# Performance work log

Measured on AMD Instinct MI355X. Metric: run time of the kernel, lower is better.

## Reference

```python
import jax, jax.numpy as jnp
import numpy as np

LN_EPS = 1e-5
TOP_K = 2

def _layer_norm(x, g, b):
    m = jnp.mean(x, axis=-1, keepdims=True)
    v = jnp.var(x, axis=-1, keepdims=True)
    return (x - m) * jax.lax.rsqrt(v + LN_EPS) * g + b

def _skew(X, pad_value):
    # shift every row one step right: [B,M,L] -> [B,M,M+L]
    B, M, L = X.shape
    X = jnp.pad(X, ((0, 0), (0, 0), (0, M + 1)), constant_values=pad_value)
    X = X.reshape(B, -1)[:, :-M]
    return X.reshape(B, M, M + L)

def _unskew(X):
    # reverse of _skew: [B,M,M+L] -> [B,M,L]
    B, M, Lt = X.shape
    L = Lt - M
    X = X.reshape(B, -1)
    X = jnp.pad(X, ((0, 0), (0, M)))
    return X.reshape(B, M, M + L + 1)[:, :, :L]

def _heads(x, K, D):
    # [B,T,H] -> [B*K,T,D]
    B, T, _ = x.shape
    return x.reshape(B, T, K, D).transpose(0, 2, 1, 3).reshape(B * K, T, D)

def setup_inputs() -> dict:
    key = jax.random.key(0)
    ks = jax.random.split(key, 12)
    B, M, L, H, Dh, E, Kh = 4, 512, 512, 1024, 2048, 8, 8
    D = H // Kh
    s = 0.02
    return {
        "h": jax.random.normal(ks[0], (B, M, H), jnp.float32),
        "h_cache": jax.random.normal(ks[1], (B, L, H), jnp.float32),
        "key_pe": jax.random.normal(ks[2], (1, D, L), jnp.float32) * s,
        "Wq": jax.random.normal(ks[3], (H, H), jnp.float32) * s,
        "Wk": jax.random.normal(ks[4], (H, H), jnp.float32) * s,
        "Wv": jax.random.normal(ks[5], (H, H), jnp.float32) * s,
        "Wo": jax.random.normal(ks[6], (H, H), jnp.float32) * s,
        "ln1_g": jnp.ones((H,), jnp.float32),
        "ln1_b": jnp.zeros((H,), jnp.float32),
        "gate_W": jax.random.normal(ks[7], (H, E), jnp.float32) * s,
        "gate_b": jnp.zeros((E,), jnp.float32),
        "W1": jax.random.normal(ks[8], (E, H, Dh), jnp.float32) * s,
        "b1": jnp.zeros((E, Dh), jnp.float32),
        "W2": jax.random.normal(ks[9], (E, Dh, H), jnp.float32) * s,
        "b2": jnp.zeros((E, H), jnp.float32),
        "ln2_g": jnp.ones((H,), jnp.float32),
        "ln2_b": jnp.zeros((H,), jnp.float32),
    }

def reference(h, h_cache, key_pe, Wq, Wk, Wv, Wo, ln1_g, ln1_b,
              gate_W, gate_b, W1, b1, W2, b2, ln2_g, ln2_b):
    B, M, H = h.shape
    L = h_cache.shape[1]
    Kh = 8
    D = H // Kh
    # --- multi-head relative-position attention over (cache, current) ---
    h_all = jnp.concatenate([h_cache, h], axis=1)            # [B, L+M, H]
    q = _heads(h @ Wq, Kh, D)                                # [B*K, M, D]
    k = _heads(h_all @ Wk, Kh, D)                            # [B*K, M+L, D]
    v = _heads(h_all @ Wv, Kh, D)                            # [B*K, M+L, D]
    attn_cont = _unskew(jnp.einsum('bmd,bnd->bmn', q, k))    # [B*K, M, L]
    attn_pos = jnp.einsum('bmd,xdl->bml', q, key_pe)         # [B*K, M, L]
    attn = jax.nn.softmax((attn_cont + attn_pos) / jnp.sqrt(jnp.float32(D)), axis=-1)
    out = jnp.einsum('bmn,bnd->bmd', _skew(attn, 0.0), v)    # [B*K, M, D]
    out = out.reshape(B, Kh, M, D).transpose(0, 2, 1, 3).reshape(B, M, H)
    attn_out = out @ Wo
    h1 = _layer_norm(h + attn_out, ln1_g, ln1_b)             # post-LN residual
    # --- top-k gated MoE FFN (NaiveGate), post-LN residual ---
    x = h1.reshape(-1, H)                                    # [N, H]
    N = x.shape[0]
    E = gate_b.shape[0]
    logits = x @ gate_W + gate_b                             # [N, E]
    top_val, top_idx = jax.lax.top_k(logits, TOP_K)          # [N, k]
    scores = jax.nn.softmax(top_val, axis=-1)                # [N, k]
    combine = jnp.zeros((N, E), x.dtype).at[jnp.arange(N)[:, None], top_idx].add(scores)
    he = jax.nn.relu(jnp.einsum('nh,ehf->enf', x, W1) + b1[:, None, :])  # [E, N, Dh]
    ye = jnp.einsum('enf,efh->enh', he, W2) + b2[:, None, :]             # [E, N, H]
    core = jnp.einsum('ne,enh->nh', combine, ye).reshape(B, M, H)
    output = _layer_norm(h1 + core, ln2_g, ln2_b)
    return output, top_idx
```

## Files before the change

### kernel.cpp

```cpp
#include <hip/hip_runtime.h>
#include <hip/hip_bf16.h>
#include <stdint.h>


typedef _Float16 f16;
typedef _Float16 f16x8 __attribute__((ext_vector_type(8)));
typedef _Float16 f16x4 __attribute__((ext_vector_type(4)));
typedef float    f32x4 __attribute__((ext_vector_type(4)));
typedef int      i32x4 __attribute__((ext_vector_type(4)));

#define MFMA16(a, b, c) __builtin_amdgcn_mfma_f32_16x16x32_f16((a), (b), (c), 0, 0, 0)
#define LO_SCALE 2048.0f
#define LO_INV   4.8828125e-4f

__device__ __forceinline__ void split2(float x, f16* h, f16* l) {
  f16 hh = (f16)x;
  *h = hh;
  *l = (f16)((x - (float)hh) * LO_SCALE);
}

__device__ __forceinline__ f32x4 zero4() {
  f32x4 z; z[0] = 0.f; z[1] = 0.f; z[2] = 0.f; z[3] = 0.f; return z;
}

__device__ __forceinline__ void gload_lds16(const void* g, void* l) {
  __builtin_amdgcn_global_load_lds((__attribute__((address_space(1))) void*)g,
                                   (__attribute__((address_space(3))) void*)l,
                                   16, 0, 0);
}

__global__ void __launch_bounds__(256) cast_hall_k(const float* __restrict__ h,
                                                   const float* __restrict__ hc,
                                                   f16* __restrict__ hi,
                                                   f16* __restrict__ lo) {
  int c = blockIdx.x * 256 + threadIdx.x;
  int e0 = c * 8;
  int row = e0 >> 10;
  int col = e0 & 1023;
  int b = row >> 10, pos = row & 1023;
  const float* src = (pos < 512) ? (hc + (size_t)((b << 9) + pos) * 1024 + col)
                                 : (h  + (size_t)((b << 9) + (pos - 512)) * 1024 + col);
  float4 v0 = ((const float4*)src)[0];
  float4 v1 = ((const float4*)src)[1];
  float xs[8] = {v0.x, v0.y, v0.z, v0.w, v1.x, v1.y, v1.z, v1.w};
  f16x8 vh, vl;
#pragma unroll
  for (int i = 0; i < 8; i++) { f16 a, bb; split2(xs[i], &a, &bb); vh[i] = a; vl[i] = bb; }
  *(f16x8*)&hi[e0] = vh;
  *(f16x8*)&lo[e0] = vl;
}

template <int SPLIT>
__global__ void __launch_bounds__(256) wprep_k(const float* __restrict__ in,
                                               f16* __restrict__ oh,
                                               f16* __restrict__ ol,
                                               int K, int N) {
  in += (size_t)blockIdx.z * K * N;
  oh += (size_t)blockIdx.z * K * N;
  if constexpr (SPLIT) ol += (size_t)blockIdx.z * K * N;
  __shared__ float tile[32][33];
  const int n0 = blockIdx.x * 32, k0 = blockIdx.y * 32;
  {
    int r = threadIdx.x >> 3, c4 = (threadIdx.x & 7) * 4;
    float4 v = *(const float4*)&in[(size_t)(k0 + r) * N + n0 + c4];
    tile[r][c4 + 0] = v.x; tile[r][c4 + 1] = v.y;
    tile[r][c4 + 2] = v.z; tile[r][c4 + 3] = v.w;
  }
  __syncthreads();
  int t = threadIdx.x;
  if constexpr (!SPLIT) { if (t >= 128) return; }
  int half = SPLIT ? (t >> 7) : 0;
  int r = t & 127;
  int nt = r >> 6, lane = r & 63;
  int lr = lane & 15, lgp = lane >> 4;
  f16x8 v;
#pragma unroll
  for (int j = 0; j < 8; j++) {
    float x = tile[lgp * 8 + j][nt * 16 + lr];
    f16 hh, ll; split2(x, &hh, &ll);
    v[j] = half ? ll : hh;
  }
  size_t blob = (((size_t)(n0 >> 4) + nt) * (K >> 5) + (k0 >> 5)) * 512 + lane * 8;
  f16* dst = half ? ol : oh;
  *(f16x8*)&dst[blob] = v;
}

template <int SPLIT>
__global__ void __launch_bounds__(256) transpose_cast_k(const float* __restrict__ in,
                                                        f16* __restrict__ oh,
                                                        f16* __restrict__ ol,
                                                        int R, int C) {
  in += (size_t)blockIdx.z * R * C;
  oh += (size_t)blockIdx.z * R * C;
  if constexpr (SPLIT) ol += (size_t)blockIdx.z * R * C;
  __shared__ float tile[32][33];
  int c0 = blockIdx.x * 32, r0 = blockIdx.y * 32;
  int tr = threadIdx.x >> 3, tc = (threadIdx.x & 7) * 4;
  float4 v = *(const float4*)&in[(size_t)(r0 + tr) * C + c0 + tc];
  tile[tr][tc + 0] = v.x; tile[tr][tc + 1] = v.y; tile[tr][tc + 2] = v.z; tile[tr][tc + 3] = v.w;
  __syncthreads();
  int oc = tr;
  int orr = tc;
  f16x4 vh, vl;
#pragma unroll
  for (int i = 0; i < 4; i++) {
    float x = tile[orr + i][oc];
    f16 a, bb; split2(x, &a, &bb);
    vh[i] = a; vl[i] = bb;
  }
  *(f16x4*)&oh[(size_t)(c0 + oc) * R + r0 + orr] = vh;
  if constexpr (SPLIT) *(f16x4*)&ol[(size_t)(c0 + oc) * R + r0 + orr] = vl;
}

#define AM_ID 0
#define AM_GA 2
#define AM_PA 3
#define EP_QKV 0
#define EP_F32 2
#define EP_HE 3
#define EP_YE 4

template <int SPLIT, int BM, int BN, int AMAP, int EPI>
__global__ void __launch_bounds__(256) gemm_k(
    const f16* __restrict__ Ah, const f16* __restrict__ Al,
    const f16* __restrict__ Bh, const f16* __restrict__ Bl,
    void* __restrict__ o0, void* __restrict__ o1,
    const float* __restrict__ bias,
    int Kd, int strideA, int bExpStride,
    const int* __restrict__ list, const int* __restrict__ bases,
    const int* __restrict__ counts) {
  constexpr int PL = SPLIT ? 2 : 1;
  constexpr int MT = BM / 32;
  constexpr int NT = BN / 32;
  constexpr int AIT = BM / 64;
  const int e = blockIdx.z;
  int cnt = 0, base0 = 0;
  if constexpr (AMAP == AM_GA || AMAP == AM_PA) {
    cnt = counts[e]; base0 = bases[e];
    if ((int)blockIdx.y * BM >= cnt) return;
    Bh += (size_t)e * bExpStride;
    if constexpr (SPLIT) Bl += (size_t)e * bExpStride;
  }
  __shared__ f16 sA[PL][BM * 32];
  const int n0 = blockIdx.x * BN, r0 = blockIdx.y * BM;
  const int tid = threadIdx.x, lane = tid & 63, wv = tid >> 6;
  const int wm = (wv >> 1) * (BM / 2), wn = (wv & 1) * (BN / 2);
  const int bKt = Kd >> 5;
  const int gnt0 = (n0 + wn) >> 4;

  f32x4 accM[MT][NT], accC[MT][NT];
#pragma unroll
  for (int i = 0; i < MT; i++)
#pragma unroll
    for (int j = 0; j < NT; j++) { accM[i][j] = zero4(); accC[i][j] = zero4(); }

  int aRow[AIT], aCu[AIT];
#pragma unroll
  for (int c = 0; c < AIT; c++) {
    int u = c * 256 + tid;
    int r = u >> 2, cu = u & 3;
    aCu[c] = ((cu ^ ((r >> 1) & 3)) << 3);
    int rr = r0 + r;
    int g;
    if constexpr (AMAP == AM_ID) g = rr;
    else if constexpr (AMAP == AM_GA) g = (rr < cnt) ? list[base0 + rr] : 0;
    else g = base0 + rr;
    aRow[c] = g;
  }

  for (int k0 = 0; k0 < Kd; k0 += 32) {
    const int kt = k0 >> 5;
    f16x8 bh[NT], bl[NT];
#pragma unroll
    for (int nt = 0; nt < NT; nt++) {
      size_t bi = ((size_t)(gnt0 + nt) * bKt + kt) * 512 + lane * 8;
      bh[nt] = *(const f16x8*)&Bh[bi];
      if constexpr (SPLIT) bl[nt] = *(const f16x8*)&Bl[bi];
    }
#pragma unroll
    for (int c = 0; c < AIT; c++) {
      int u = c * 256 + tid;
      gload_lds16(&Ah[(size_t)aRow[c] * strideA + k0 + aCu[c]], &sA[0][u * 8]);
      if constexpr (SPLIT)
        gload_lds16(&Al[(size_t)aRow[c] * strideA + k0 + aCu[c]], &sA[1][u * 8]);
    }
    __syncthreads();

    f16x8 ah[MT], al[MT];
#pragma unroll
    for (int mt = 0; mt < MT; mt++) {
      int r = wm + mt * 16 + (lane & 15);
      int cu = (lane >> 4) ^ ((r >> 1) & 3);
      ah[mt] = *(const f16x8*)&sA[0][(r * 4 + cu) * 8];
      if constexpr (SPLIT) al[mt] = *(const f16x8*)&sA[1][(r * 4 + cu) * 8];
    }
#pragma unroll
    for (int nt = 0; nt < NT; nt++) {
#pragma unroll
      for (int mt = 0; mt < MT; mt++) {
        accM[mt][nt] = MFMA16(ah[mt], bh[nt], accM[mt][nt]);
        if constexpr (SPLIT) {
          accC[mt][nt] = MFMA16(ah[mt], bl[nt], accC[mt][nt]);
          accC[mt][nt] = MFMA16(al[mt], bh[nt], accC[mt][nt]);
        }
      }
    }
    __syncthreads();
  }

#pragma unroll
  for (int mt = 0; mt < MT; mt++)
#pragma unroll
    for (int nt = 0; nt < NT; nt++)
#pragma unroll
      for (int rg = 0; rg < 4; rg++) {
        int row = r0 + wm + mt * 16 + ((lane >> 4) << 2) + rg;
        int col = n0 + wn + nt * 16 + (lane & 15);
        float v = accM[mt][nt][rg];
        if constexpr (SPLIT) v += accC[mt][nt][rg] * LO_INV;
        if constexpr (EPI == EP_QKV) {
          f16* QH = (f16*)o0;
          f16* QL = QH + (1u << 21);
          f16* KH = QL + (1u << 21);
          f16* KL = KH + (1u << 22);
          f16* VTH = KL + (1u << 22);
          f16* VTL = VTH + (1u << 22);
          int b = row >> 10, pos = row & 1023;
          int seg = col >> 10, hd = (col >> 7) & 7, d = col & 127;
          f16 hh, ll; split2(v, &hh, &ll);
          if (seg == 0) {
            if (pos >= 512) {
              size_t ad = ((size_t)((((b << 3) + hd) << 9) + (pos - 512))) * 128 + d;
              QH[ad] = hh; QL[ad] = ll;
            }
          } else if (seg == 1) {
            size_t ad = ((size_t)((((b << 3) + hd) << 10) + pos)) * 128 + d;
            KH[ad] = hh; KL[ad] = ll;
          } else {
            size_t ad = ((size_t)((((b << 3) + hd) << 7) + d)) * 1024 + pos;
            VTH[ad] = hh; VTL[ad] = ll;
          }
        } else if constexpr (EPI == EP_F32) {
          ((float*)o0)[(size_t)row * 1024 + col] = v;
        } else if constexpr (EPI == EP_HE) {
          if (row < cnt) {
            float t = v + bias[(e << 11) + col];
            ((f16*)o0)[(size_t)(base0 + row) * 2048 + col] = (f16)fmaxf(t, 0.f);
          }
        } else if constexpr (EPI == EP_YE) {
          if (row < cnt)
            ((float*)o0)[(size_t)(base0 + row) * 1024 + col] = v + bias[(e << 10) + col];
        }
      }
}

__device__ __forceinline__ void unpack_p(const unsigned* sp, f16x8* hi, f16x8* lo) {
  i32x4 u0 = *(const i32x4*)sp;
  i32x4 u1 = *(const i32x4*)(sp + 4);
  i32x4 h, l;
  h[0] = (u0[0] & 0xffff) | (u0[1] << 16);
  h[1] = (u0[2] & 0xffff) | (u0[3] << 16);
  h[2] = (u1[0] & 0xffff) | (u1[1] << 16);
  h[3] = (u1[2] & 0xffff) | (u1[3] << 16);
  l[0] = (int)(((unsigned)u0[0] >> 16) | ((unsigned)u0[1] & 0xffff0000u));
  l[1] = (int)(((unsigned)u0[2] >> 16) | ((unsigned)u0[3] & 0xffff0000u));
  l[2] = (int)(((unsigned)u1[0] >> 16) | ((unsigned)u1[1] & 0xffff0000u));
  l[3] = (int)(((unsigned)u1[2] >> 16) | ((unsigned)u1[3] & 0xffff0000u));
  *hi = __builtin_bit_cast(f16x8, h);
  *lo = __builtin_bit_cast(f16x8, l);
}

__global__ void __launch_bounds__(256) attn_k(
    const f16* __restrict__ qh_, const f16* __restrict__ ql_,
    const f16* __restrict__ kh_, const f16* __restrict__ kl_,
    const f16* __restrict__ ph_, const f16* __restrict__ pl_,
    const f16* __restrict__ vh_, const f16* __restrict__ vl_,
    f16* __restrict__ oh_, f16* __restrict__ ol_) {
  __shared__ float S[32][548];
  const int bh = blockIdx.y;
  const int m0 = blockIdx.x * 32;
  const int tid = threadIdx.x, lane = tid & 63, wv = tid >> 6;
  const int lr = lane & 15, lgp = lane >> 4;

  f16x8 qh[2][4], ql[2][4];
  {
    const size_t qbase = ((size_t)bh * 512 + m0) * 128;
#pragma unroll
    for (int mt = 0; mt < 2; mt++)
#pragma unroll
      for (int kb = 0; kb < 4; kb++) {
        size_t off = qbase + (size_t)(mt * 16 + lr) * 128 + kb * 32 + lgp * 8;
        qh[mt][kb] = *(const f16x8*)&qh_[off];
        ql[mt][kb] = *(const f16x8*)&ql_[off];
      }
  }

  {
    const size_t kbase = ((size_t)bh * 1024 + m0) * 128;
    int ntB = (wv < 2) ? wv * 9 : 18 + (wv - 2) * 8;
    int ntE = ntB + ((wv < 2) ? 9 : 8);
    for (int nt = ntB; nt < ntE; ++nt) {
      f16x8 kh[4], kl[4];
#pragma unroll
      for (int kb = 0; kb < 4; kb++) {
        size_t off = kbase + (size_t)(nt * 16 + lr) * 128 + kb * 32 + lgp * 8;
        kh[kb] = *(const f16x8*)&kh_[off];
        kl[kb] = *(const f16x8*)&kl_[off];
      }
      f32x4 aM[2], aC[2];
      aM[0] = zero4(); aM[1] = zero4(); aC[0] = zero4(); aC[1] = zero4();
#pragma unroll
      for (int kb = 0; kb < 4; kb++)
#pragma unroll
        for (int mt = 0; mt < 2; mt++) {
          aM[mt] = MFMA16(qh[mt][kb], kh[kb], aM[mt]);
          aC[mt] = MFMA16(qh[mt][kb], kl[kb], aC[mt]);
          aC[mt] = MFMA16(ql[mt][kb], kh[kb], aC[mt]);
        }
#pragma unroll
      for (int mt = 0; mt < 2; mt++)
#pragma unroll
        for (int rg = 0; rg < 4; rg++) {
          int m = mt * 16 + lgp * 4 + rg;
          S[m][nt * 16 + lr] = aM[mt][rg] + aC[mt][rg] * LO_INV;
        }
    }
  }
  __syncthreads();

  {
    for (int lt = wv * 8; lt < wv * 8 + 8; ++lt) {
      f16x8 eh[4], el[4];
#pragma unroll
      for (int kb = 0; kb < 4; kb++) {
        size_t off = (size_t)(lt * 16 + lr) * 128 + kb * 32 + lgp * 8;
        eh[kb] = *(const f16x8*)&ph_[off];
        el[kb] = *(const f16x8*)&pl_[off];
      }
      f32x4 aM[2], aC[2];
      aM[0] = zero4(); aM[1] = zero4(); aC[0] = zero4(); aC[1] = zero4();
#pragma unroll
      for (int kb = 0; kb < 4; kb++)
#pragma unroll
        for (int mt = 0; mt < 2; mt++) {
          aM[mt] = MFMA16(qh[mt][kb], eh[kb], aM[mt]);
          aC[mt] = MFMA16(qh[mt][kb], el[kb], aC[mt]);
          aC[mt] = MFMA16(ql[mt][kb], eh[kb], aC[mt]);
        }
#pragma unroll
      for (int mt = 0; mt < 2; mt++)
#pragma unroll
        for (int rg = 0; rg < 4; rg++) {
          int m = mt * 16 + lgp * 4 + rg;
          int lc = lt * 16 + lr;
          S[m][m + lc] += aM[mt][rg] + aC[mt][rg] * LO_INV;
        }
    }
  }
  __syncthreads();

  {
    const float scl = 0.08838834764831843f;
    for (int rr = 0; rr < 8; ++rr) {
      int m = wv * 8 + rr;
      float mx = -3.0e38f;
#pragma unroll
      for (int it = 0; it < 9; ++it) {
        int j = it * 64 + lane;
        if (j < 544 && j >= m && j < m + 512) mx = fmaxf(mx, S[m][j]);
      }
#pragma unroll
      for (int o = 32; o > 0; o >>= 1) mx = fmaxf(mx, __shfl_xor(mx, o));
      float pv[9]; float sm = 0.f;
#pragma unroll
      for (int it = 0; it < 9; ++it) {
        int j = it * 64 + lane;
        float p = 0.f;
        if (j < 544 && j >= m && j < m + 512) p = expf((S[m][j] - mx) * scl);
        pv[it] = p; sm += p;
      }
#pragma unroll
      for (int o = 32; o > 0; o >>= 1) sm += __shfl_xor(sm, o);
      float inv = 1.0f / sm;
#pragma unroll
      for (int it = 0; it < 9; ++it) {
        int j = it * 64 + lane;
        if (j < 544) {
          float pn = pv[it] * inv;
          f16 hh, ll; split2(pn, &hh, &ll);
          unsigned pk = (unsigned)__builtin_bit_cast(unsigned short, hh) |
                        ((unsigned)__builtin_bit_cast(unsigned short, ll) << 16);
          ((unsigned*)&S[m][0])[j] = pk;
        }
      }
    }
  }
  __syncthreads();

  f32x4 accM[2][2], accC[2][2];
#pragma unroll
  for (int i = 0; i < 2; i++)
#pragma unroll
    for (int j = 0; j < 2; j++) { accM[i][j] = zero4(); accC[i][j] = zero4(); }
  for (int kb = 0; kb < 17; ++kb) {
    f16x8 pah[2], pal[2];
#pragma unroll
    for (int mt = 0; mt < 2; mt++) {
      const unsigned* sp = (const unsigned*)&S[mt * 16 + lr][0] + kb * 32 + lgp * 8;
      unpack_p(sp, &pah[mt], &pal[mt]);
    }
#pragma unroll
    for (int ntl = 0; ntl < 2; ++ntl) {
      int d = wv * 32 + ntl * 16 + lr;
      size_t off = ((size_t)bh * 128 + d) * 1024 + m0 + kb * 32 + lgp * 8;
      f16x8 vh = *(const f16x8*)&vh_[off];
      f16x8 vl = *(const f16x8*)&vl_[off];
#pragma unroll
      for (int mt = 0; mt < 2; mt++) {
        accM[mt][ntl] = MFMA16(pah[mt], vh, accM[mt][ntl]);
        accC[mt][ntl] = MFMA16(pah[mt], vl, accC[mt][ntl]);
        accC[mt][ntl] = MFMA16(pal[mt], vh, accC[mt][ntl]);
      }
    }
  }
  const int b = bh >> 3, hd = bh & 7;
#pragma unroll
  for (int mt = 0; mt < 2; mt++)
#pragma unroll
    for (int ntl = 0; ntl < 2; ntl++)
#pragma unroll
      for (int rg = 0; rg < 4; rg++) {
        int m = mt * 16 + lgp * 4 + rg;
        int d = wv * 32 + ntl * 16 + lr;
        float v = accM[mt][ntl][rg] + accC[mt][ntl][rg] * LO_INV;
        size_t ad = ((size_t)(b * 512 + m0 + m)) * 1024 + hd * 128 + d;
        f16 hh, ll; split2(v, &hh, &ll);
        oh_[ad] = hh; ol_[ad] = ll;
      }
}

__device__ __forceinline__ float blk_sum(float v, float* red) {
#pragma unroll
  for (int o = 32; o > 0; o >>= 1) v += __shfl_xor(v, o);
  int wv = threadIdx.x >> 6;
  if ((threadIdx.x & 63) == 0) red[wv] = v;
  __syncthreads();
  float r = red[0] + red[1] + red[2] + red[3];
  __syncthreads();
  return r;
}

__global__ void __launch_bounds__(256) ln1_k(const float* __restrict__ h,
                                             const float* __restrict__ ap,
                                             const float* __restrict__ g,
                                             const float* __restrict__ bb,
                                             float* __restrict__ h1,
                                             f16* __restrict__ h1h) {
  int row = blockIdx.x;
  __shared__ float red[4];
  float4 hv = ((const float4*)(h + (size_t)row * 1024))[threadIdx.x];
  float4 av = ((const float4*)(ap + (size_t)row * 1024))[threadIdx.x];
  float4 x; x.x = hv.x + av.x; x.y = hv.y + av.y; x.z = hv.z + av.z; x.w = hv.w + av.w;
  float s = x.x + x.y + x.z + x.w;
  s = blk_sum(s, red);
  float mean = s * (1.0f / 1024.0f);
  float4 d; d.x = x.x - mean; d.y = x.y - mean; d.z = x.z - mean; d.w = x.w - mean;
  float s2 = d.x * d.x + d.y * d.y + d.z * d.z + d.w * d.w;
  s2 = blk_sum(s2, red);
  float var = s2 * (1.0f / 1024.0f);
  float inv = 1.0f / sqrtf(var + 1e-5f);
  float4 gv = ((const float4*)g)[threadIdx.x];
  float4 bv = ((const float4*)bb)[threadIdx.x];
  float4 y; y.x = d.x * inv * gv.x + bv.x; y.y = d.y * inv * gv.y + bv.y;
  y.z = d.z * inv * gv.z + bv.z; y.w = d.w * inv * gv.w + bv.w;
  ((float4*)(h1 + (size_t)row * 1024))[threadIdx.x] = y;
  f16x4 yh; yh[0] = (f16)y.x; yh[1] = (f16)y.y; yh[2] = (f16)y.z; yh[3] = (f16)y.w;
  *(f16x4*)&h1h[(size_t)row * 1024 + threadIdx.x * 4] = yh;
}

__global__ void __launch_bounds__(256) gate_k(const float* __restrict__ h1,
                                              const float* __restrict__ gW,
                                              const float* __restrict__ gb,
                                              float* __restrict__ outIdx,
                                              float* __restrict__ sc,
                                              int* __restrict__ te,
                                              int* __restrict__ ctrl) {
  int t = blockIdx.x * 4 + (threadIdx.x >> 6);
  int lane = threadIdx.x & 63;
  float a0 = 0, a1 = 0, a2 = 0, a3 = 0, a4 = 0, a5 = 0, a6 = 0, a7 = 0;
  for (int i = lane; i < 1024; i += 64) {
    float x = h1[(size_t)t * 1024 + i];
    const float4* w = (const float4*)&gW[i * 8];
    float4 w0 = w[0], w1 = w[1];
    a0 += x * w0.x; a1 += x * w0.y; a2 += x * w0.z; a3 += x * w0.w;
    a4 += x * w1.x; a5 += x * w1.y; a6 += x * w1.z; a7 += x * w1.w;
  }
  float av[8] = {a0, a1, a2, a3, a4, a5, a6, a7};
#pragma unroll
  for (int e = 0; e < 8; e++)
#pragma unroll
    for (int o = 32; o > 0; o >>= 1) av[e] += __shfl_xor(av[e], o);
  if (lane == 0) {
#pragma unroll
    for (int e = 0; e < 8; e++) av[e] += gb[e];
    int i0 = 0; float v0 = av[0];
#pragma unroll
    for (int e = 1; e < 8; e++) if (av[e] > v0) { v0 = av[e]; i0 = e; }
    int i1 = -1; float v1 = -3.0e38f;
#pragma unroll
    for (int e = 0; e < 8; e++) if (e != i0 && av[e] > v1) { v1 = av[e]; i1 = e; }
    float ex = expf(v1 - v0);
    float den = 1.0f + ex;
    outIdx[t * 2] = (float)i0; outIdx[t * 2 + 1] = (float)i1;
    sc[t * 2] = 1.0f / den; sc[t * 2 + 1] = ex / den;
    te[t * 2] = i0; te[t * 2 + 1] = i1;
    atomicAdd(&ctrl[i0], 1); atomicAdd(&ctrl[i1], 1);
  }
}

__global__ void scan_k(int* ctrl) {
  if (threadIdx.x == 0 && blockIdx.x == 0) {
    int s = 0;
    for (int e = 0; e < 8; e++) { ctrl[8 + e] = s; s += ctrl[e]; }
  }
}

__global__ void __launch_bounds__(256) scatter_k(const int* __restrict__ te,
                                                 int* ctrl,
                                                 int* __restrict__ list,
                                                 int* __restrict__ ppos) {
  int t = blockIdx.x * 256 + threadIdx.x;
  if (t >= 2048) return;
#pragma unroll
  for (int s = 0; s < 2; s++) {
    int e = te[t * 2 + s];
    int pos = atomicAdd(&ctrl[16 + e], 1);
    int pr = ctrl[8 + e] + pos;
    list[pr] = t;
    ppos[t * 2 + s] = pr;
  }
}

__global__ void __launch_bounds__(256) comb_ln2_k(const float* __restrict__ h1,
                                                  const float* __restrict__ ye,
                                                  const float* __restrict__ sc,
                                                  const int* __restrict__ ppos,
                                                  const float* __restrict__ g,
                                                  const float* __restrict__ bb,
                                                  float* __restrict__ out) {
  int row = blockIdx.x;
  __shared__ float red[4];
  int p0 = ppos[row * 2], p1 = ppos[row * 2 + 1];
  float s0 = sc[row * 2], s1 = sc[row * 2 + 1];
  float4 a = ((const float4*)(h1 + (size_t)row * 1024))[threadIdx.x];
  float4 y0 = ((const float4*)(ye + (size_t)p0 * 1024))[threadIdx.x];
  float4 y1 = ((const float4*)(ye + (size_t)p1 * 1024))[threadIdx.x];
  float4 x;
  x.x = a.x + s0 * y0.x + s1 * y1.x; x.y = a.y + s0 * y0.y + s1 * y1.y;
  x.z = a.z + s0 * y0.z + s1 * y1.z; x.w = a.w + s0 * y0.w + s1 * y1.w;
  float s = x.x + x.y + x.z + x.w;
  s = blk_sum(s, red);
  float mean = s * (1.0f / 1024.0f);
  float4 d; d.x = x.x - mean; d.y = x.y - mean; d.z = x.z - mean; d.w = x.w - mean;
  float s2 = d.x * d.x + d.y * d.y + d.z * d.z + d.w * d.w;
  s2 = blk_sum(s2, red);
  float var = s2 * (1.0f / 1024.0f);
  float inv = 1.0f / sqrtf(var + 1e-5f);
  float4 gv = ((const float4*)g)[threadIdx.x];
  float4 bv = ((const float4*)bb)[threadIdx.x];
  float4 y; y.x = d.x * inv * gv.x + bv.x; y.y = d.y * inv * gv.y + bv.y;
  y.z = d.z * inv * gv.z + bv.z; y.w = d.w * inv * gv.w + bv.w;
  ((float4*)(out + (size_t)row * 1024))[threadIdx.x] = y;
}

extern "C" void kernel_launch(void* const* d_in, const int* in_sizes, int n_in,
                              void* d_out, int out_size, void* d_ws, size_t ws_size,
                              hipStream_t stream) {
  const float* h   = (const float*)d_in[0];
  const float* hc  = (const float*)d_in[1];
  const float* pe  = (const float*)d_in[2];
  const float* Wq  = (const float*)d_in[3];
  const float* Wk  = (const float*)d_in[4];
  const float* Wv  = (const float*)d_in[5];
  const float* Wo  = (const float*)d_in[6];
  const float* g1  = (const float*)d_in[7];
  const float* b1n = (const float*)d_in[8];
  const float* gW  = (const float*)d_in[9];
  const float* gb  = (const float*)d_in[10];
  const float* W1  = (const float*)d_in[11];
  const float* b1e = (const float*)d_in[12];
  const float* W2  = (const float*)d_in[13];
  const float* b2e = (const float*)d_in[14];
  const float* g2  = (const float*)d_in[15];
  const float* b2n = (const float*)d_in[16];
  float* out = (float*)d_out;
  float* outIdx = out + 2097152;

  char* w = (char*)d_ws;
  size_t off = 0;
  auto alloc = [&](size_t bytes) -> char* {
    char* p = w + off;
    off += (bytes + 255) & ~(size_t)255;
    return p;
  };
  int*   ctrl    = (int*)alloc(128);
  f16*   hallH   = (f16*)alloc(4096ull * 1024 * 2);
  f16*   hallL   = (f16*)alloc(4096ull * 1024 * 2);
  f16*   WqkvtH  = (f16*)alloc(3072ull * 1024 * 2);
  f16*   WqkvtL  = (f16*)alloc(3072ull * 1024 * 2);
  f16*   WotH    = (f16*)alloc(1024ull * 1024 * 2);
  f16*   WotL    = (f16*)alloc(1024ull * 1024 * 2);
  f16*   peH     = (f16*)alloc(512ull * 128 * 2);
  f16*   peL     = (f16*)alloc(512ull * 128 * 2);
  f16*   qkv     = (f16*)alloc(20971520ull * 2);
  f16*   qH  = qkv;
  f16*   qL  = qH + (1u << 21);
  f16*   kH  = qL + (1u << 21);
  f16*   kL  = kH + (1u << 22);
  f16*   vtH = kL + (1u << 22);
  f16*   vtL = vtH + (1u << 22);
  f16*   attH  = (f16*)alloc(2097152ull * 2);
  f16*   attL  = (f16*)alloc(2097152ull * 2);
  float* aproj = (float*)alloc(2097152ull * 4);
  float* h1    = (float*)alloc(2097152ull * 4);
  f16*   h1h   = (f16*)alloc(2097152ull * 2);
  f16*   W1t   = (f16*)alloc(16777216ull * 2);
  f16*   W2t   = (f16*)alloc(16777216ull * 2);
  f16*   he    = (f16*)alloc(4224ull * 2048 * 2);
  float* ye    = (float*)alloc(4224ull * 1024 * 4);
  float* scb   = (float*)alloc(2048ull * 2 * 4);
  int*   te    = (int*)alloc(2048ull * 2 * 4);
  int*   ppos  = (int*)alloc(2048ull * 2 * 4);
  int*   list  = (int*)alloc(4096ull * 4);
  (void)in_sizes; (void)n_in; (void)out_size; (void)ws_size;

  hipMemsetAsync(ctrl, 0, 128, stream);

  cast_hall_k<<<2048, 256, 0, stream>>>(h, hc, hallH, hallL);
  wprep_k<1><<<dim3(32, 32, 1), 256, 0, stream>>>(Wq, WqkvtH, WqkvtL, 1024, 1024);
  wprep_k<1><<<dim3(32, 32, 1), 256, 0, stream>>>(Wk, WqkvtH + 1048576, WqkvtL + 1048576, 1024, 1024);
  wprep_k<1><<<dim3(32, 32, 1), 256, 0, stream>>>(Wv, WqkvtH + 2097152, WqkvtL + 2097152, 1024, 1024);
  wprep_k<1><<<dim3(32, 32, 1), 256, 0, stream>>>(Wo, WotH, WotL, 1024, 1024);
  transpose_cast_k<1><<<dim3(16, 4, 1), 256, 0, stream>>>(pe, peH, peL, 128, 512);
  wprep_k<0><<<dim3(64, 32, 8), 256, 0, stream>>>(W1, W1t, nullptr, 1024, 2048);
  wprep_k<0><<<dim3(32, 64, 8), 256, 0, stream>>>(W2, W2t, nullptr, 2048, 1024);

  gemm_k<1, 128, 64, AM_ID, EP_QKV><<<dim3(48, 32, 1), 256, 0, stream>>>(
      hallH, hallL, WqkvtH, WqkvtL, qkv, nullptr, nullptr, 1024, 1024, 0,
      nullptr, nullptr, nullptr);

  attn_k<<<dim3(16, 32, 1), 256, 0, stream>>>(qH, qL, kH, kL, peH, peL, vtH, vtL, attH, attL);

  gemm_k<1, 64, 64, AM_ID, EP_F32><<<dim3(16, 32, 1), 256, 0, stream>>>(
      attH, attL, WotH, WotL, aproj, nullptr, nullptr, 1024, 1024, 0,
      nullptr, nullptr, nullptr);
  ln1_k<<<2048, 256, 0, stream>>>(h, aproj, g1, b1n, h1, h1h);

  gate_k<<<512, 256, 0, stream>>>(h1, gW, gb, outIdx, scb, te, ctrl);
  scan_k<<<1, 64, 0, stream>>>(ctrl);
  scatter_k<<<8, 256, 0, stream>>>(te, ctrl, list, ppos);

  gemm_k<0, 64, 128, AM_GA, EP_HE><<<dim3(16, 32, 8), 256, 0, stream>>>(
      h1h, nullptr, W1t, nullptr, he, nullptr, b1e, 1024, 1024, 2048 * 1024,
      list, ctrl + 8, ctrl);
  gemm_k<0, 64, 128, AM_PA, EP_YE><<<dim3(8, 32, 8), 256, 0, stream>>>(
      he, nullptr, W2t, nullptr, ye, nullptr, b2e, 2048, 2048, 1024 * 2048,
      nullptr, ctrl + 8, ctrl);

  comb_ln2_k<<<2048, 256, 0, stream>>>(h1, ye, scb, ppos, g2, b2n, out);
}
```

Baseline: 665.0 us.

## Double-buffer A tiles in LDS and prefetch B fragments in GEMM mainloop

Converts the GEMM k-loop from a single-buffered load-sync-compute-sync pattern to a two-stage ping-pong pipeline. The next k-tile of A is issued to a second LDS buffer, and the next B fragments are loaded into registers, while MFMAs run on the current buffer. This drops one barrier per k-step and is meant to hide global load latency. In exchange it doubles the LDS footprint and adds B register pressure, which may reduce occupancy.

Measured after the change: 653.4 us. Within noise of the previous version (-1.7%).

```diff
diff --git a/kernel.cpp b/kernel.cpp
--- a/kernel.cpp
+++ b/kernel.cpp
@@ -141,7 +141,7 @@
     Bh += (size_t)e * bExpStride;
     if constexpr (SPLIT) Bl += (size_t)e * bExpStride;
   }
-  __shared__ f16 sA[PL][BM * 32];
+  __shared__ f16 sA[2][PL][BM * 32];
   const int n0 = blockIdx.x * BN, r0 = blockIdx.y * BM;
   const int tid = threadIdx.x, lane = tid & 63, wv = tid >> 6;
   const int wm = (wv >> 1) * (BM / 2), wn = (wv & 1) * (BN / 2);
@@ -168,31 +168,32 @@
     aRow[c] = g;
   }
 
-  for (int k0 = 0; k0 < Kd; k0 += 32) {
-    const int kt = k0 >> 5;
-    f16x8 bh[NT], bl[NT];
+  auto STAGE = [&](int buf, int kt) {
+    int k0 = kt << 5;
+#pragma unroll
+    for (int c = 0; c < AIT; c++) {
+      int u = c * 256 + tid;
+      gload_lds16(&Ah[(size_t)aRow[c] * strideA + k0 + aCu[c]], &sA[buf][0][u * 8]);
+      if constexpr (SPLIT)
+        gload_lds16(&Al[(size_t)aRow[c] * strideA + k0 + aCu[c]], &sA[buf][1][u * 8]);
+    }
+  };
+  auto LOADB = [&](f16x8 (&bh)[NT], f16x8 (&bl)[NT], int kt) {
 #pragma unroll
     for (int nt = 0; nt < NT; nt++) {
       size_t bi = ((size_t)(gnt0 + nt) * bKt + kt) * 512 + lane * 8;
       bh[nt] = *(const f16x8*)&Bh[bi];
       if constexpr (SPLIT) bl[nt] = *(const f16x8*)&Bl[bi];
     }
-#pragma unroll
-    for (int c = 0; c < AIT; c++) {
-      int u = c * 256 + tid;
-      gload_lds16(&Ah[(size_t)aRow[c] * strideA + k0 + aCu[c]], &sA[0][u * 8]);
-      if constexpr (SPLIT)
-        gload_lds16(&Al[(size_t)aRow[c] * strideA + k0 + aCu[c]], &sA[1][u * 8]);
-    }
-    __syncthreads();
-
+  };
+  auto COMPUTE = [&](int buf, f16x8 (&bh)[NT], f16x8 (&bl)[NT]) {
     f16x8 ah[MT], al[MT];
 #pragma unroll
     for (int mt = 0; mt < MT; mt++) {
       int r = wm + mt * 16 + (lane & 15);
       int cu = (lane >> 4) ^ ((r >> 1) & 3);
-      ah[mt] = *(const f16x8*)&sA[0][(r * 4 + cu) * 8];
-      if constexpr (SPLIT) al[mt] = *(const f16x8*)&sA[1][(r * 4 + cu) * 8];
+      ah[mt] = *(const f16x8*)&sA[buf][0][(r * 4 + cu) * 8];
+      if constexpr (SPLIT) al[mt] = *(const f16x8*)&sA[buf][1][(r * 4 + cu) * 8];
     }
 #pragma unroll
     for (int nt = 0; nt < NT; nt++) {
@@ -205,7 +206,24 @@
         }
       }
     }
+  };
+
+  f16x8 b0h[NT], b0l[NT], b1h[NT], b1l[NT];
+  const int nkt = Kd >> 5;
+
+  STAGE(0, 0);
+  LOADB(b0h, b0l, 0);
+  __syncthreads();
+
+  for (int kt = 0; kt < nkt; kt += 2) {
+    if (kt + 1 < nkt) { STAGE(1, kt + 1); LOADB(b1h, b1l, kt + 1); }
+    COMPUTE(0, b0h, b0l);
     __syncthreads();
+    if (kt + 1 < nkt) {
+      if (kt + 2 < nkt) { STAGE(0, kt + 2); LOADB(b0h, b0l, kt + 2); }
+      COMPUTE(1, b1h, b1l);
+      __syncthreads();
+    }
   }
 
 #pragma unroll
```
